# Kernel optimization log

Measured on AMD Instinct MI355X. Metric: run time of the kernel, lower is better.

## Reference

```python
import jax, jax.numpy as jnp
import numpy as np

OFFSET_SCALE = 6.0
S = 256
N = S * S  # 65536 UV grid points


def setup_inputs() -> dict:
    key = jax.random.key(0)
    k1, k2, k3, k4 = jax.random.split(key, 4)
    B = 64
    Offset = jax.random.normal(k1, (B, 3, S, S), dtype=jnp.float32)
    Posmap_kpt = jax.random.normal(k2, (B, 3, S, S), dtype=jnp.float32)
    mean_posmap = jax.random.normal(k3, (3, S, S), dtype=jnp.float32)
    uv_kpt = jax.random.randint(k4, (68, 2), 0, S, dtype=jnp.int32)
    return {"Offset": Offset, "Posmap_kpt": Posmap_kpt,
            "mean_posmap": mean_posmap, "uv_kpt": uv_kpt}


def reference(Offset, Posmap_kpt, mean_posmap, uv_kpt):
    B = Offset.shape[0]
    # offsetmap / kptmap: NCHW -> NHWC
    offsetmap = jnp.transpose(Offset * OFFSET_SCALE + mean_posmap[None], (0, 2, 3, 1))  # [B,256,256,3]
    kptmap = jnp.transpose(Posmap_kpt, (0, 2, 3, 1))                                    # [B,256,256,3]

    kpt_dst = kptmap[:, uv_kpt[:, 0], uv_kpt[:, 1]]     # [B,68,3]
    kpt_src = offsetmap[:, uv_kpt[:, 0], uv_kpt[:, 1]]  # [B,68,3]
    offsetflat = offsetmap.reshape(B, N, 3)

    # 16 quadruples of consecutive keypoints: (x, x+1, x+2, x+3) for x in 0,4,...,60
    quad = (jnp.arange(0, 64, 4)[:, None] + jnp.arange(4)[None, :])  # [16,4]
    p = kpt_src[:, quad]  # [B,16,4,3]
    q = kpt_dst[:, quad]  # [B,16,4,3]

    # Batched closed-form rigid fit: A = p0 - p{1,2,3}, Bm = q0 - q{1,2,3}
    A = p[:, :, 0:1, :] - p[:, :, 1:, :]   # [B,16,3,3]
    Bm = q[:, :, 0:1, :] - q[:, :, 1:, :]  # [B,16,3,3]
    R = jnp.linalg.inv(A) @ Bm             # [B,16,3,3]
    T = jnp.mean(q - p @ R, axis=-2)       # [B,16,3]

    # Coarse rotation -> yaw -> keypoint visibility
    R_coarse = jnp.mean(R, axis=1)  # [B,3,3]
    yaw = jnp.arctan2(-R_coarse[:, 2, 0],
                      jnp.sqrt(R_coarse[:, 0, 0] ** 2 + R_coarse[:, 1, 0] ** 2))
    yaw_rate = yaw / jnp.pi
    left = jnp.maximum(yaw_rate * S, 0.0)        # [B]
    right = jnp.minimum(S + yaw_rate * S, float(S))  # [B]
    col = uv_kpt[:, 1].astype(jnp.float32)       # [68]
    vis = jnp.where((col[None, :] <= left[:, None]) | (col[None, :] >= right[:, None]),
                    0.001, 1.0)                  # [B,68]

    # Visibility-weighted average of per-quad transforms
    w = jnp.prod(vis[:, quad], axis=-1)          # [B,16]
    s = jnp.sum(w, axis=1)                       # [B]
    R_p = jnp.einsum('bq,bqij->bij', w, R) / s[:, None, None]  # [B,3,3]
    T_p = jnp.einsum('bq,bqi->bi', w, T) / s[:, None]          # [B,3]

    out = offsetflat @ R_p + T_p[:, None, :]     # [B,65536,3]
    return jnp.transpose(out.reshape(B, S, S, 3), (0, 3, 1, 2))  # [B,3,256,256]
```

## Files before the change

### kernel.cpp

```cpp
#include <hip/hip_runtime.h>
#include <math.h>

#define S 256
#define NPIX (S * S)
#define B 64
#define NQUAD 16

__global__ __launch_bounds__(64) void pose_solve_kernel(
    const float* __restrict__ Offset,
    const float* __restrict__ Posmap,
    const float* __restrict__ meanp,
    const int*   __restrict__ uv,
    float*       __restrict__ params)
{
    const int b = blockIdx.x;
    const int t = threadIdx.x;

    __shared__ double sp[64][3];
    __shared__ double sq[64][3];
    __shared__ double sR[NQUAD][9];
    __shared__ double sT[NQUAD][3];
    __shared__ int    scol[64];

    {
        const int u = uv[2 * t + 0];
        const int v = uv[2 * t + 1];
        scol[t] = v;
        const int n = u * S + v;
        const float* offb = Offset + (size_t)b * 3 * NPIX;
        const float* posb = Posmap + (size_t)b * 3 * NPIX;
#pragma unroll
        for (int c = 0; c < 3; ++c) {
            sp[t][c] = (double)offb[c * NPIX + n] * 6.0 + (double)meanp[c * NPIX + n];
            sq[t][c] = (double)posb[c * NPIX + n];
        }
    }
    __syncthreads();

    if (t < NQUAD) {
        const int k0 = 4 * t;
        double A[3][3], Bm[3][3];
#pragma unroll
        for (int r = 0; r < 3; ++r)
#pragma unroll
            for (int c = 0; c < 3; ++c) {
                A[r][c]  = sp[k0][c] - sp[k0 + 1 + r][c];
                Bm[r][c] = sq[k0][c] - sq[k0 + 1 + r][c];
            }
        const double c00 = A[1][1] * A[2][2] - A[1][2] * A[2][1];
        const double c01 = A[1][2] * A[2][0] - A[1][0] * A[2][2];
        const double c02 = A[1][0] * A[2][1] - A[1][1] * A[2][0];
        const double det = A[0][0] * c00 + A[0][1] * c01 + A[0][2] * c02;
        const double id  = 1.0 / det;
        double inv[3][3];
        inv[0][0] = c00 * id;
        inv[0][1] = (A[0][2] * A[2][1] - A[0][1] * A[2][2]) * id;
        inv[0][2] = (A[0][1] * A[1][2] - A[0][2] * A[1][1]) * id;
        inv[1][0] = c01 * id;
        inv[1][1] = (A[0][0] * A[2][2] - A[0][2] * A[2][0]) * id;
        inv[1][2] = (A[0][2] * A[1][0] - A[0][0] * A[1][2]) * id;
        inv[2][0] = c02 * id;
        inv[2][1] = (A[0][1] * A[2][0] - A[0][0] * A[2][1]) * id;
        inv[2][2] = (A[0][0] * A[1][1] - A[0][1] * A[1][0]) * id;

        double R[3][3];
#pragma unroll
        for (int i = 0; i < 3; ++i)
#pragma unroll
            for (int j = 0; j < 3; ++j) {
                R[i][j] = inv[i][0] * Bm[0][j] + inv[i][1] * Bm[1][j] + inv[i][2] * Bm[2][j];
                sR[t][i * 3 + j] = R[i][j];
            }
#pragma unroll
        for (int c = 0; c < 3; ++c) {
            double acc = 0.0;
#pragma unroll
            for (int j = 0; j < 4; ++j) {
                const double pr = sp[k0 + j][0] * R[0][c] +
                                  sp[k0 + j][1] * R[1][c] +
                                  sp[k0 + j][2] * R[2][c];
                acc += sq[k0 + j][c] - pr;
            }
            sT[t][c] = acc * 0.25;
        }
    }
    __syncthreads();

    if (t == 0) {
        double r00 = 0.0, r10 = 0.0, r20 = 0.0;
        for (int q = 0; q < NQUAD; ++q) {
            r00 += sR[q][0];
            r10 += sR[q][3];
            r20 += sR[q][6];
        }
        r00 /= NQUAD; r10 /= NQUAD; r20 /= NQUAD;
        const double yaw = atan2(-r20, sqrt(r00 * r00 + r10 * r10));
        const double yr  = yaw / M_PI;
        const double left  = fmax(yr * (double)S, 0.0);
        const double right = fmin((double)S + yr * (double)S, (double)S);

        double w[NQUAD];
        double s = 0.0;
        for (int q = 0; q < NQUAD; ++q) {
            double wq = 1.0;
#pragma unroll
            for (int j = 0; j < 4; ++j) {
                const double col = (double)scol[4 * q + j];
                const double vis = (col <= left || col >= right) ? 0.001 : 1.0;
                wq *= vis;
            }
            w[q] = wq;
            s += wq;
        }
        double Rp[9] = {0, 0, 0, 0, 0, 0, 0, 0, 0};
        double Tp[3] = {0, 0, 0};
        for (int q = 0; q < NQUAD; ++q) {
#pragma unroll
            for (int e = 0; e < 9; ++e) Rp[e] += w[q] * sR[q][e];
#pragma unroll
            for (int e = 0; e < 3; ++e) Tp[e] += w[q] * sT[q][e];
        }
        float* pb = params + b * 12;
        const double sinv = 1.0 / s;
#pragma unroll
        for (int e = 0; e < 9; ++e) pb[e] = (float)(Rp[e] * sinv);
#pragma unroll
        for (int e = 0; e < 3; ++e) pb[9 + e] = (float)(Tp[e] * sinv);
    }
}

__global__ __launch_bounds__(256) void apply_pose_kernel(
    const float* __restrict__ Offset,
    const float* __restrict__ meanp,
    const float* __restrict__ params,
    float*       __restrict__ out)
{
    const int tid = blockIdx.x * 256 + threadIdx.x;
    const int b   = tid >> 14;
    const int n   = (tid & 16383) << 2;

    const float* pb = params + b * 12;
    const float r00 = pb[0], r01 = pb[1], r02 = pb[2];
    const float r10 = pb[3], r11 = pb[4], r12 = pb[5];
    const float r20 = pb[6], r21 = pb[7], r22 = pb[8];
    const float t0 = pb[9], t1 = pb[10], t2 = pb[11];

    const float* offb = Offset + (size_t)b * 3 * NPIX;
    const float4 o0 = *(const float4*)(offb + 0 * NPIX + n);
    const float4 o1 = *(const float4*)(offb + 1 * NPIX + n);
    const float4 o2 = *(const float4*)(offb + 2 * NPIX + n);
    const float4 m0 = *(const float4*)(meanp + 0 * NPIX + n);
    const float4 m1 = *(const float4*)(meanp + 1 * NPIX + n);
    const float4 m2 = *(const float4*)(meanp + 2 * NPIX + n);

    float4 x, y, z;
    x.x = fmaf(o0.x, 6.f, m0.x); x.y = fmaf(o0.y, 6.f, m0.y);
    x.z = fmaf(o0.z, 6.f, m0.z); x.w = fmaf(o0.w, 6.f, m0.w);
    y.x = fmaf(o1.x, 6.f, m1.x); y.y = fmaf(o1.y, 6.f, m1.y);
    y.z = fmaf(o1.z, 6.f, m1.z); y.w = fmaf(o1.w, 6.f, m1.w);
    z.x = fmaf(o2.x, 6.f, m2.x); z.y = fmaf(o2.y, 6.f, m2.y);
    z.z = fmaf(o2.z, 6.f, m2.z); z.w = fmaf(o2.w, 6.f, m2.w);

    float4 u, v, wv;
    u.x = fmaf(x.x, r00, fmaf(y.x, r10, fmaf(z.x, r20, t0)));
    u.y = fmaf(x.y, r00, fmaf(y.y, r10, fmaf(z.y, r20, t0)));
    u.z = fmaf(x.z, r00, fmaf(y.z, r10, fmaf(z.z, r20, t0)));
    u.w = fmaf(x.w, r00, fmaf(y.w, r10, fmaf(z.w, r20, t0)));
    v.x = fmaf(x.x, r01, fmaf(y.x, r11, fmaf(z.x, r21, t1)));
    v.y = fmaf(x.y, r01, fmaf(y.y, r11, fmaf(z.y, r21, t1)));
    v.z = fmaf(x.z, r01, fmaf(y.z, r11, fmaf(z.z, r21, t1)));
    v.w = fmaf(x.w, r01, fmaf(y.w, r11, fmaf(z.w, r21, t1)));
    wv.x = fmaf(x.x, r02, fmaf(y.x, r12, fmaf(z.x, r22, t2)));
    wv.y = fmaf(x.y, r02, fmaf(y.y, r12, fmaf(z.y, r22, t2)));
    wv.z = fmaf(x.z, r02, fmaf(y.z, r12, fmaf(z.z, r22, t2)));
    wv.w = fmaf(x.w, r02, fmaf(y.w, r12, fmaf(z.w, r22, t2)));

    float* outb = out + (size_t)b * 3 * NPIX;
    *(float4*)(outb + 0 * NPIX + n) = u;
    *(float4*)(outb + 1 * NPIX + n) = v;
    *(float4*)(outb + 2 * NPIX + n) = wv;
}

extern "C" void kernel_launch(void* const* d_in, const int* in_sizes, int n_in,
                              void* d_out, int out_size, void* d_ws, size_t ws_size,
                              hipStream_t stream) {
    const float* Offset = (const float*)d_in[0];
    const float* Posmap = (const float*)d_in[1];
    const float* meanp  = (const float*)d_in[2];
    const int*   uv     = (const int*)d_in[3];
    float* out = (float*)d_out;
    float* params = (float*)d_ws;

    pose_solve_kernel<<<B, 64, 0, stream>>>(Offset, Posmap, meanp, uv, params);

    const int threads_total = B * (NPIX / 4);
    apply_pose_kernel<<<threads_total / 256, 256, 0, stream>>>(Offset, meanp, params, out);
}
```

Baseline: 135.2 us.

## Fuse pose solve into apply kernel, recomputing params per block

```diff
diff --git a/kernel.cpp b/kernel.cpp
--- a/kernel.cpp
+++ b/kernel.cpp
@@ -5,29 +5,43 @@
 #define NPIX (S * S)
 #define B 64
 #define NQUAD 16
-
-__global__ __launch_bounds__(64) void pose_solve_kernel(
+#define BLK_PER_BATCH 32
+#define GPB 512
+
+__global__ __launch_bounds__(256) void visible_rebuild_fused(
     const float* __restrict__ Offset,
     const float* __restrict__ Posmap,
     const float* __restrict__ meanp,
     const int*   __restrict__ uv,
-    float*       __restrict__ params)
+    float*       __restrict__ out)
 {
-    const int b = blockIdx.x;
-    const int t = threadIdx.x;
-
     __shared__ double sp[64][3];
     __shared__ double sq[64][3];
     __shared__ double sR[NQUAD][9];
     __shared__ double sT[NQUAD][3];
     __shared__ int    scol[64];
-
-    {
+    __shared__ float  sprm[12];
+
+    const int bk = blockIdx.x;
+    const int b  = bk >> 5;
+    const int jb = bk & (BLK_PER_BATCH - 1);
+    const int t  = threadIdx.x;
+
+    const float* offb = Offset + (size_t)b * 3 * NPIX;
+
+    const int n0 = (jb * GPB + t) << 2;
+    const float4 o0a = *(const float4*)(offb  + 0 * NPIX + n0);
+    const float4 o1a = *(const float4*)(offb  + 1 * NPIX + n0);
+    const float4 o2a = *(const float4*)(offb  + 2 * NPIX + n0);
+    const float4 m0a = *(const float4*)(meanp + 0 * NPIX + n0);
+    const float4 m1a = *(const float4*)(meanp + 1 * NPIX + n0);
+    const float4 m2a = *(const float4*)(meanp + 2 * NPIX + n0);
+
+    if (t < 64) {
         const int u = uv[2 * t + 0];
         const int v = uv[2 * t + 1];
         scol[t] = v;
         const int n = u * S + v;
-        const float* offb = Offset + (size_t)b * 3 * NPIX;
         const float* posb = Posmap + (size_t)b * 3 * NPIX;
 #pragma unroll
         for (int c = 0; c < 3; ++c) {
@@ -106,8 +120,7 @@
 #pragma unroll
             for (int j = 0; j < 4; ++j) {
                 const double col = (double)scol[4 * q + j];
-                const double vis = (col <= left || col >= right) ? 0.001 : 1.0;
-                wq *= vis;
+                wq *= (col <= left || col >= right) ? 0.001 : 1.0;
             }
             w[q] = wq;
             s += wq;
@@ -120,65 +133,83 @@
 #pragma unroll
             for (int e = 0; e < 3; ++e) Tp[e] += w[q] * sT[q][e];
         }
-        float* pb = params + b * 12;
         const double sinv = 1.0 / s;
 #pragma unroll
-        for (int e = 0; e < 9; ++e) pb[e] = (float)(Rp[e] * sinv);
-#pragma unroll
-        for (int e = 0; e < 3; ++e) pb[9 + e] = (float)(Tp[e] * sinv);
-    }
-}
-
-__global__ __launch_bounds__(256) void apply_pose_kernel(
-    const float* __restrict__ Offset,
-    const float* __restrict__ meanp,
-    const float* __restrict__ params,
-    float*       __restrict__ out)
-{
-    const int tid = blockIdx.x * 256 + threadIdx.x;
-    const int b   = tid >> 14;
-    const int n   = (tid & 16383) << 2;
-
-    const float* pb = params + b * 12;
-    const float r00 = pb[0], r01 = pb[1], r02 = pb[2];
-    const float r10 = pb[3], r11 = pb[4], r12 = pb[5];
-    const float r20 = pb[6], r21 = pb[7], r22 = pb[8];
-    const float t0 = pb[9], t1 = pb[10], t2 = pb[11];
-
-    const float* offb = Offset + (size_t)b * 3 * NPIX;
-    const float4 o0 = *(const float4*)(offb + 0 * NPIX + n);
-    const float4 o1 = *(const float4*)(offb + 1 * NPIX + n);
-    const float4 o2 = *(const float4*)(offb + 2 * NPIX + n);
-    const float4 m0 = *(const float4*)(meanp + 0 * NPIX + n);
-    const float4 m1 = *(const float4*)(meanp + 1 * NPIX + n);
-    const float4 m2 = *(const float4*)(meanp + 2 * NPIX + n);
-
-    float4 x, y, z;
-    x.x = fmaf(o0.x, 6.f, m0.x); x.y = fmaf(o0.y, 6.f, m0.y);
-    x.z = fmaf(o0.z, 6.f, m0.z); x.w = fmaf(o0.w, 6.f, m0.w);
-    y.x = fmaf(o1.x, 6.f, m1.x); y.y = fmaf(o1.y, 6.f, m1.y);
-    y.z = fmaf(o1.z, 6.f, m1.z); y.w = fmaf(o1.w, 6.f, m1.w);
-    z.x = fmaf(o2.x, 6.f, m2.x); z.y = fmaf(o2.y, 6.f, m2.y);
-    z.z = fmaf(o2.z, 6.f, m2.z); z.w = fmaf(o2.w, 6.f, m2.w);
-
-    float4 u, v, wv;
-    u.x = fmaf(x.x, r00, fmaf(y.x, r10, fmaf(z.x, r20, t0)));
-    u.y = fmaf(x.y, r00, fmaf(y.y, r10, fmaf(z.y, r20, t0)));
-    u.z = fmaf(x.z, r00, fmaf(y.z, r10, fmaf(z.z, r20, t0)));
-    u.w = fmaf(x.w, r00, fmaf(y.w, r10, fmaf(z.w, r20, t0)));
-    v.x = fmaf(x.x, r01, fmaf(y.x, r11, fmaf(z.x, r21, t1)));
-    v.y = fmaf(x.y, r01, fmaf(y.y, r11, fmaf(z.y, r21, t1)));
-    v.z = fmaf(x.z, r01, fmaf(y.z, r11, fmaf(z.z, r21, t1)));
-    v.w = fmaf(x.w, r01, fmaf(y.w, r11, fmaf(z.w, r21, t1)));
-    wv.x = fmaf(x.x, r02, fmaf(y.x, r12, fmaf(z.x, r22, t2)));
-    wv.y = fmaf(x.y, r02, fmaf(y.y, r12, fmaf(z.y, r22, t2)));
-    wv.z = fmaf(x.z, r02, fmaf(y.z, r12, fmaf(z.z, r22, t2)));
-    wv.w = fmaf(x.w, r02, fmaf(y.w, r12, fmaf(z.w, r22, t2)));
-
+        for (int e = 0; e < 9; ++e) sprm[e] = (float)(Rp[e] * sinv);
+#pragma unroll
+        for (int e = 0; e < 3; ++e) sprm[9 + e] = (float)(Tp[e] * sinv);
+    }
+    __syncthreads();
+
+    const float r00 = sprm[0], r01 = sprm[1], r02 = sprm[2];
+    const float r10 = sprm[3], r11 = sprm[4], r12 = sprm[5];
+    const float r20 = sprm[6], r21 = sprm[7], r22 = sprm[8];
+    const float t0 = sprm[9], t1 = sprm[10], t2 = sprm[11];
     float* outb = out + (size_t)b * 3 * NPIX;
-    *(float4*)(outb + 0 * NPIX + n) = u;
-    *(float4*)(outb + 1 * NPIX + n) = v;
-    *(float4*)(outb + 2 * NPIX + n) = wv;
+
+    {
+        float4 x, y, z;
+        x.x = fmaf(o0a.x, 6.f, m0a.x); x.y = fmaf(o0a.y, 6.f, m0a.y);
+        x.z = fmaf(o0a.z, 6.f, m0a.z); x.w = fmaf(o0a.w, 6.f, m0a.w);
+        y.x = fmaf(o1a.x, 6.f, m1a.x); y.y = fmaf(o1a.y, 6.f, m1a.y);
+        y.z = fmaf(o1a.z, 6.f, m1a.z); y.w = fmaf(o1a.w, 6.f, m1a.w);
+        z.x = fmaf(o2a.x, 6.f, m2a.x); z.y = fmaf(o2a.y, 6.f, m2a.y);
+        z.z = fmaf(o2a.z, 6.f, m2a.z); z.w = fmaf(o2a.w, 6.f, m2a.w);
+
+        float4 u, v, wv;
+        u.x = fmaf(x.x, r00, fmaf(y.x, r10, fmaf(z.x, r20, t0)));
+        u.y = fmaf(x.y, r00, fmaf(y.y, r10, fmaf(z.y, r20, t0)));
+        u.z = fmaf(x.z, r00, fmaf(y.z, r10, fmaf(z.z, r20, t0)));
+        u.w = fmaf(x.w, r00, fmaf(y.w, r10, fmaf(z.w, r20, t0)));
+        v.x = fmaf(x.x, r01, fmaf(y.x, r11, fmaf(z.x, r21, t1)));
+        v.y = fmaf(x.y, r01, fmaf(y.y, r11, fmaf(z.y, r21, t1)));
+        v.z = fmaf(x.z, r01, fmaf(y.z, r11, fmaf(z.z, r21, t1)));
+        v.w = fmaf(x.w, r01, fmaf(y.w, r11, fmaf(z.w, r21, t1)));
+        wv.x = fmaf(x.x, r02, fmaf(y.x, r12, fmaf(z.x, r22, t2)));
+        wv.y = fmaf(x.y, r02, fmaf(y.y, r12, fmaf(z.y, r22, t2)));
+        wv.z = fmaf(x.z, r02, fmaf(y.z, r12, fmaf(z.z, r22, t2)));
+        wv.w = fmaf(x.w, r02, fmaf(y.w, r12, fmaf(z.w, r22, t2)));
+
+        *(float4*)(outb + 0 * NPIX + n0) = u;
+        *(float4*)(outb + 1 * NPIX + n0) = v;
+        *(float4*)(outb + 2 * NPIX + n0) = wv;
+    }
+
+    {
+        const int n1 = n0 + (256 << 2);
+        const float4 o0 = *(const float4*)(offb  + 0 * NPIX + n1);
+        const float4 o1 = *(const float4*)(offb  + 1 * NPIX + n1);
+        const float4 o2 = *(const float4*)(offb  + 2 * NPIX + n1);
+        const float4 m0 = *(const float4*)(meanp + 0 * NPIX + n1);
+        const float4 m1 = *(const float4*)(meanp + 1 * NPIX + n1);
+        const float4 m2 = *(const float4*)(meanp + 2 * NPIX + n1);
+
+        float4 x, y, z;
+        x.x = fmaf(o0.x, 6.f, m0.x); x.y = fmaf(o0.y, 6.f, m0.y);
+        x.z = fmaf(o0.z, 6.f, m0.z); x.w = fmaf(o0.w, 6.f, m0.w);
+        y.x = fmaf(o1.x, 6.f, m1.x); y.y = fmaf(o1.y, 6.f, m1.y);
+        y.z = fmaf(o1.z, 6.f, m1.z); y.w = fmaf(o1.w, 6.f, m1.w);
+        z.x = fmaf(o2.x, 6.f, m2.x); z.y = fmaf(o2.y, 6.f, m2.y);
+        z.z = fmaf(o2.z, 6.f, m2.z); z.w = fmaf(o2.w, 6.f, m2.w);
+
+        float4 u, v, wv;
+        u.x = fmaf(x.x, r00, fmaf(y.x, r10, fmaf(z.x, r20, t0)));
+        u.y = fmaf(x.y, r00, fmaf(y.y, r10, fmaf(z.y, r20, t0)));
+        u.z = fmaf(x.z, r00, fmaf(y.z, r10, fmaf(z.z, r20, t0)));
+        u.w = fmaf(x.w, r00, fmaf(y.w, r10, fmaf(z.w, r20, t0)));
+        v.x = fmaf(x.x, r01, fmaf(y.x, r11, fmaf(z.x, r21, t1)));
+        v.y = fmaf(x.y, r01, fmaf(y.y, r11, fmaf(z.y, r21, t1)));
+        v.z = fmaf(x.z, r01, fmaf(y.z, r11, fmaf(z.z, r21, t1)));
+        v.w = fmaf(x.w, r01, fmaf(y.w, r11, fmaf(z.w, r21, t1)));
+        wv.x = fmaf(x.x, r02, fmaf(y.x, r12, fmaf(z.x, r22, t2)));
+        wv.y = fmaf(x.y, r02, fmaf(y.y, r12, fmaf(z.y, r22, t2)));
+        wv.z = fmaf(x.z, r02, fmaf(y.z, r12, fmaf(z.z, r22, t2)));
+        wv.w = fmaf(x.w, r02, fmaf(y.w, r12, fmaf(z.w, r22, t2)));
+
+        *(float4*)(outb + 0 * NPIX + n1) = u;
+        *(float4*)(outb + 1 * NPIX + n1) = v;
+        *(float4*)(outb + 2 * NPIX + n1) = wv;
+    }
 }
 
 extern "C" void kernel_launch(void* const* d_in, const int* in_sizes, int n_in,
@@ -189,10 +220,7 @@
     const float* meanp  = (const float*)d_in[2];
     const int*   uv     = (const int*)d_in[3];
     float* out = (float*)d_out;
-    float* params = (float*)d_ws;
-
-    pose_solve_kernel<<<B, 64, 0, stream>>>(Offset, Posmap, meanp, uv, params);
-
-    const int threads_total = B * (NPIX / 4);
-    apply_pose_kernel<<<threads_total / 256, 256, 0, stream>>>(Offset, meanp, params, out);
+
+    visible_rebuild_fused<<<B * BLK_PER_BATCH, 256, 0, stream>>>(
+        Offset, Posmap, meanp, uv, out);
 }
```

Result: slower. 177.4 us (+31.2%).
